# Performance work log

Measured on AMD Instinct MI355X. Metric: run time of the kernel, lower is better.

## Reference

```python
import jax, jax.numpy as jnp
import numpy as np

T, B, F, H, O = 512, 1024, 16, 32, 8  # seq_len, batch, input_size, hidden, classes


def setup_inputs() -> dict:
    key = jax.random.key(0)
    ks = jax.random.split(key, 11)
    s = 1.0 / np.sqrt(H)  # PyTorch LSTM/Linear uniform init scale
    u = lambda k, shp: jax.random.uniform(k, shp, jnp.float32, -s, s)
    return {
        "x": jax.random.normal(ks[0], (T, B, F), jnp.float32),
        "W_ih_f": u(ks[1], (4 * H, F)),
        "W_hh_f": u(ks[2], (4 * H, H)),
        "b_f": u(ks[3], (4 * H,)),  # combined b_ih + b_hh
        "W_ih_b": u(ks[4], (4 * H, F)),
        "W_hh_b": u(ks[5], (4 * H, H)),
        "b_b": u(ks[6], (4 * H,)),
        "W_fc_h": u(ks[7], (O, 2 * H)),
        "b_fc_h": u(ks[8], (O,)),
        "W_fc_o": jax.random.uniform(ks[9], (O, B * O), jnp.float32, -1 / np.sqrt(B * O), 1 / np.sqrt(B * O)),
        "b_fc_o": u(ks[10], (O,)),
    }


def _lstm_final_hidden(x, W_ih, W_hh, b):
    """Run one LSTM direction over x:(T,B,F); return final hidden h:(B,H)."""
    h_dim = W_hh.shape[1]
    # precompute input contribution for all timesteps: (T, B, 4H)
    gates_x = jnp.einsum('tbf,gf->tbg', x, W_ih) + b

    def step(carry, gx):
        h, c = carry
        g = gx + h @ W_hh.T  # (B, 4H), PyTorch gate order i,f,g,o
        i, f, gg, o = jnp.split(g, 4, axis=-1)
        c = jax.nn.sigmoid(f) * c + jax.nn.sigmoid(i) * jnp.tanh(gg)
        h = jax.nn.sigmoid(o) * jnp.tanh(c)
        return (h, c), None

    bsz = x.shape[1]
    init = (jnp.zeros((bsz, h_dim), x.dtype), jnp.zeros((bsz, h_dim), x.dtype))
    (h, _), _ = jax.lax.scan(step, init, gates_x)
    return h


def reference(x, W_ih_f, W_hh_f, b_f, W_ih_b, W_hh_b, b_b,
              W_fc_h, b_fc_h, W_fc_o, b_fc_o):
    h_fwd = _lstm_final_hidden(x, W_ih_f, W_hh_f, b_f)          # hidden_state[-2]
    h_bwd = _lstm_final_hidden(x[::-1], W_ih_b, W_hh_b, b_b)    # hidden_state[-1]
    hidden = jnp.concatenate([h_fwd, h_bwd], axis=1)            # (B, 2H)
    hidden_fc = hidden @ W_fc_h.T + b_fc_h                      # (B, O)
    flat = hidden_fc.reshape(-1)                                # (B*O,) == flat_dim
    out = W_fc_o @ flat + b_fc_o                                # (O,)
    return jax.nn.softmax(out)
```

## Files before the change

kernel.cpp:

```cpp
#include <hip/hip_runtime.h>

#define TT 512
#define BB 1024
#define FF 16
#define HH 32
#define OO 8
#define CH 16
#define NC (TT / CH)
#define NG 128

typedef _Float16 f16;
typedef f16 v2h __attribute__((ext_vector_type(2)));
typedef f16 v4h __attribute__((ext_vector_type(4)));
typedef f16 v8h __attribute__((ext_vector_type(8)));
typedef float f32x4 __attribute__((ext_vector_type(4)));
typedef int   v2i  __attribute__((ext_vector_type(2)));

__device__ __forceinline__ float rcp_fast(float x) { return __builtin_amdgcn_rcpf(x); }
__device__ __forceinline__ float sigm2(float y) {
    return rcp_fast(1.0f + __builtin_amdgcn_exp2f(-y));
}
__device__ __forceinline__ float fdot2(v2h a, v2h b, float c) {
    return __builtin_amdgcn_fdot2(a, b, c, false);
}
__device__ __forceinline__ v2h i2h(int s) { return __builtin_bit_cast(v2h, s); }

__device__ __forceinline__ float xhalf_swap(float v) {
#if __has_builtin(__builtin_amdgcn_permlane32_swap)
    int pi = __float_as_int(v);
    v2i sw = __builtin_amdgcn_permlane32_swap(pi, pi, false, false);
    return __int_as_float(sw.x);
#else
    return __shfl_xor(v, 32);
#endif
}

#define LSTEP(tt, S)                                                           \
  {                                                                            \
    const int xm = ((tt) & 7) << 2;                                            \
    const float gx0 = gxc##S[(tt) * NG + (r0 ^ xm)];                           \
    const float gx1 = gxc##S[(tt) * NG + (r1 ^ xm)];                           \
    float B0 = fdot2(i2h(hs##S[0]), w0h[0], pb0);                              \
    float B1 = fdot2(i2h(hs##S[0]), w1h[0], pb1);                              \
    float C0 = fdot2(i2h(hs##S[8]), w0h[8], gx0);                              \
    float C1 = fdot2(i2h(hs##S[8]), w1h[8], gx1);                              \
    _Pragma("unroll")                                                          \
    for (int j = 1; j < 8; ++j) {                                              \
      B0 = fdot2(i2h(hs##S[j]),     w0h[j],     B0);                           \
      B1 = fdot2(i2h(hs##S[j]),     w1h[j],     B1);                           \
      C0 = fdot2(i2h(hs##S[8 + j]), w0h[8 + j], C0);                           \
      C1 = fdot2(i2h(hs##S[8 + j]), w1h[8 + j], C1);                           \
    }                                                                          \
    const float g0 = B0 + C0;                                                  \
    const float g1 = B1 + C1;                                                  \
    const float s0 = sigm2(g0);                         \
    const float s1 = fmaf(sigm2(g1), pm, pa);           \
    const float prod = s0 * s1;                                                \
    const float recv = xhalf_swap(prod);                                       \
    c##S = fmaf(s0, c##S, recv);                         \
    const float th = fmaf(2.0f, sigm2(L2E2 * c##S), -1.0f);                    \
    h##S = s1 * th;                                        \
    const int hn = __builtin_amdgcn_mov_dpp(__float_as_int(h##S),              \
                                            0xB1, 0xF, 0xF, true);             \
    auto pk = __builtin_amdgcn_cvt_pkrtz(h##S, __int_as_float(hn));            \
    const int pki = __builtin_bit_cast(int, pk);                               \
    _Pragma("unroll")                                                          \
    for (int m = 0; m < HH / 2; ++m)                                           \
      hs##S[m] = __builtin_amdgcn_readlane(pki, 32 + 2 * m);                   \
  }

__global__ __launch_bounds__(64, 1)
void lstm_seq_kernel(const float* __restrict__ x,
                     const float* __restrict__ Wih_f, const float* __restrict__ Whh_f,
                     const float* __restrict__ b_f,
                     const float* __restrict__ Wih_b, const float* __restrict__ Whh_b,
                     const float* __restrict__ b_b,
                     float* __restrict__ hidden)
{
    const int bid  = blockIdx.x;
    const int dir  = bid >> 9;
    const int bbA  = (bid & 511) * 2;
    const int bbB  = bbA + 1;
    const int lane = threadIdx.x;
    const int hi   = lane >> 5;
    const int kk   = lane & 31;

    const float* __restrict__ Wih  = dir ? Wih_b : Wih_f;
    const float* __restrict__ Whh  = dir ? Whh_b : Whh_f;
    const float* __restrict__ bias = dir ? b_b   : b_f;

    const float LOG2E = 1.4426950408889634f;
    const float L2E2  = 2.0f * LOG2E;

    const int r0 = kk + hi * HH;
    const int r1 = r0 + 2 * HH;
    const float sc0 = LOG2E;
    const float sc1 = hi ? LOG2E : L2E2;
    const float pm = hi ? 1.0f : 2.0f;
    const float pa = hi ? 0.0f : -1.0f;

    v2h w0h[HH / 2], w1h[HH / 2];
#pragma unroll
    for (int q = 0; q < HH / 4; ++q) {
        float4 a = ((const float4*)(Whh + r0 * HH))[q];
        w0h[2*q]   = (v2h){(f16)(a.x * sc0), (f16)(a.y * sc0)};
        w0h[2*q+1] = (v2h){(f16)(a.z * sc0), (f16)(a.w * sc0)};
        float4 b2 = ((const float4*)(Whh + r1 * HH))[q];
        w1h[2*q]   = (v2h){(f16)(b2.x * sc1), (f16)(b2.y * sc1)};
        w1h[2*q+1] = (v2h){(f16)(b2.z * sc1), (f16)(b2.w * sc1)};
    }
    const float pb0 = bias[r0] * sc0;
    const float pb1 = bias[r1] * sc1;

    v8h awx[8];
#pragma unroll
    for (int T = 0; T < 8; ++T) {
        v8h t = {(f16)0,(f16)0,(f16)0,(f16)0,(f16)0,(f16)0,(f16)0,(f16)0};
        if (lane < 32) {
            const int gate = T * 16 + (lane & 15);
            const float sc = (gate >= 64 && gate < 96) ? L2E2 : LOG2E;
            const float* wrow = Wih + gate * FF + (lane >> 4) * 8;
#pragma unroll
            for (int j = 0; j < 8; ++j) t[j] = (f16)(wrow[j] * sc);
        }
        awx[T] = t;
    }

    __shared__ __align__(16) f16   xsbA[2 * CH * FF], xsbB[2 * CH * FF];
    __shared__ __align__(16) float gxbA[2 * CH * NG], gxbB[2 * CH * NG];

    const int sl = lane >> 2;
    const int wl = lane & 3;
    const int t0 = dir ? (TT - 1 - sl) : sl;
    const float* xpA = x + (size_t)t0 * (BB * FF) + (size_t)bbA * FF + wl * 4;
    const float* xpB = x + (size_t)t0 * (BB * FF) + (size_t)bbB * FF + wl * 4;
    const ptrdiff_t dstep = (dir ? -(ptrdiff_t)CH : (ptrdiff_t)CH) * (BB * FF);

    const int mst = lane & 15;
    const int mq  = (lane >> 4) * 4;
    const int mxr = (mst & 7) << 2;
    const int bsel = (lane & 15) * FF + (lane >> 4) * 8;

    {
        float4 fA = *(const float4*)xpA;
        float4 fB = *(const float4*)xpB;
        *(v4h*)(xsbA + sl * FF + wl * 4) =
            (v4h){(f16)fA.x, (f16)fA.y, (f16)fA.z, (f16)fA.w};
        *(v4h*)(xsbB + sl * FF + wl * 4) =
            (v4h){(f16)fB.x, (f16)fB.y, (f16)fB.z, (f16)fB.w};
    }
    xpA += dstep; xpB += dstep;
    {
        v8h bxA = {(f16)0,(f16)0,(f16)0,(f16)0,(f16)0,(f16)0,(f16)0,(f16)0};
        v8h bxB = bxA;
        if (lane < 32) { bxA = *(const v8h*)(xsbA + bsel);
                         bxB = *(const v8h*)(xsbB + bsel); }
        float* gwA = gxbA + mst * NG;
        float* gwB = gxbB + mst * NG;
#pragma unroll
        for (int T = 0; T < 8; ++T) {
            f32x4 aA = __builtin_amdgcn_mfma_f32_16x16x32_f16(
                awx[T], bxA, (f32x4){0.f, 0.f, 0.f, 0.f}, 0, 0, 0);
            f32x4 aB = __builtin_amdgcn_mfma_f32_16x16x32_f16(
                awx[T], bxB, (f32x4){0.f, 0.f, 0.f, 0.f}, 0, 0, 0);
            *(f32x4*)(gwA + ((mq + T * 16) ^ mxr)) = aA;
            *(f32x4*)(gwB + ((mq + T * 16) ^ mxr)) = aB;
        }
    }
    float4 nfA = *(const float4*)xpA;  xpA += dstep;
    float4 nfB = *(const float4*)xpB;  xpB += dstep;

    float cA = 0.0f, hA = 0.0f, cB = 0.0f, hB = 0.0f;
    int hsA[HH / 2], hsB[HH / 2];
#pragma unroll
    for (int m = 0; m < HH / 2; ++m) { hsA[m] = 0; hsB[m] = 0; }

    for (int ci = 0; ci < NC; ++ci) {
        const int bufc = ci & 1;
        const int bufn = bufc ^ 1;
        const bool more = (ci + 1 < NC);

        v8h bxA = {(f16)0,(f16)0,(f16)0,(f16)0,(f16)0,(f16)0,(f16)0,(f16)0};
        v8h bxB = bxA;
        if (more) {
            *(v4h*)(xsbA + bufn * (CH * FF) + sl * FF + wl * 4) =
                (v4h){(f16)nfA.x, (f16)nfA.y, (f16)nfA.z, (f16)nfA.w};
            *(v4h*)(xsbB + bufn * (CH * FF) + sl * FF + wl * 4) =
                (v4h){(f16)nfB.x, (f16)nfB.y, (f16)nfB.z, (f16)nfB.w};
            if (lane < 32) {
                bxA = *(const v8h*)(xsbA + bufn * (CH * FF) + bsel);
                bxB = *(const v8h*)(xsbB + bufn * (CH * FF) + bsel);
            }
            if (ci + 2 < NC) {
                nfA = *(const float4*)xpA;  xpA += dstep;
                nfB = *(const float4*)xpB;  xpB += dstep;
            }
        }

        const float* gxcA = gxbA + bufc * (CH * NG);
        const float* gxcB = gxbB + bufc * (CH * NG);

#pragma unroll
        for (int tt = 0; tt < 12; ++tt) { LSTEP(tt, A) LSTEP(tt, B) }

        if (more) {
            float* gwA = gxbA + bufn * (CH * NG) + mst * NG;
            float* gwB = gxbB + bufn * (CH * NG) + mst * NG;
#pragma unroll
            for (int T = 0; T < 8; ++T) {
                f32x4 aA = __builtin_amdgcn_mfma_f32_16x16x32_f16(
                    awx[T], bxA, (f32x4){0.f, 0.f, 0.f, 0.f}, 0, 0, 0);
                f32x4 aB = __builtin_amdgcn_mfma_f32_16x16x32_f16(
                    awx[T], bxB, (f32x4){0.f, 0.f, 0.f, 0.f}, 0, 0, 0);
                *(f32x4*)(gwA + ((mq + T * 16) ^ mxr)) = aA;
                *(f32x4*)(gwB + ((mq + T * 16) ^ mxr)) = aB;
            }
        }

#pragma unroll
        for (int tt = 12; tt < CH; ++tt) { LSTEP(tt, A) LSTEP(tt, B) }
    }

    if (hi) {
        hidden[(size_t)bbA * 64 + dir * HH + kk] = hA;
        hidden[(size_t)bbB * 64 + dir * HH + kk] = hB;
    }
}

__global__ __launch_bounds__(256)
void fc_partial_kernel(const float* __restrict__ hidden,
                       const float* __restrict__ Wfh, const float* __restrict__ bfh,
                       const float* __restrict__ Wfo,
                       float* __restrict__ partials)
{
    __shared__ float wsh[OO * 64];
    const int tid = threadIdx.x;
    for (int i = tid; i < OO * 64; i += 256) wsh[i] = Wfh[i];
    __syncthreads();

    const int r   = tid >> 3;
    const int o   = tid & 7;
    const int row = blockIdx.x * 32 + r;

    const float* hrow = hidden + (size_t)row * 64;
    float acc = bfh[o];
#pragma unroll
    for (int j = 0; j < 64; ++j) acc += hrow[j] * wsh[o * 64 + j];

    const int fidx = blockIdx.x * 256 + tid;

    float pv[OO];
#pragma unroll
    for (int o2 = 0; o2 < OO; ++o2) pv[o2] = Wfo[(size_t)o2 * (BB * OO) + fidx] * acc;

    __shared__ float red[4][OO];
#pragma unroll
    for (int o2 = 0; o2 < OO; ++o2) {
        float v = pv[o2];
        for (int off = 32; off > 0; off >>= 1) v += __shfl_down(v, off);
        if ((tid & 63) == 0) red[tid >> 6][o2] = v;
    }
    __syncthreads();
    if (tid < OO) {
        partials[blockIdx.x * OO + tid] =
            red[0][tid] + red[1][tid] + red[2][tid] + red[3][tid];
    }
}

__global__ void finalize_kernel(const float* __restrict__ partials,
                                const float* __restrict__ bfo,
                                float* __restrict__ out)
{
    __shared__ float s[OO];
    const int tid = threadIdx.x;
    if (tid < OO) {
        float acc = bfo[tid];
        for (int b = 0; b < 32; ++b) acc += partials[b * OO + tid];
        s[tid] = acc;
    }
    __syncthreads();
    if (tid == 0) {
        float m = s[0];
        for (int i = 1; i < OO; ++i) m = fmaxf(m, s[i]);
        float e[OO], sum = 0.0f;
        for (int i = 0; i < OO; ++i) { e[i] = expf(s[i] - m); sum += e[i]; }
        for (int i = 0; i < OO; ++i) out[i] = e[i] / sum;
    }
}

extern "C" void kernel_launch(void* const* d_in, const int* in_sizes, int n_in,
                              void* d_out, int out_size, void* d_ws, size_t ws_size,
                              hipStream_t stream) {
    const float* x     = (const float*)d_in[0];
    const float* Wih_f = (const float*)d_in[1];
    const float* Whh_f = (const float*)d_in[2];
    const float* b_f   = (const float*)d_in[3];
    const float* Wih_b = (const float*)d_in[4];
    const float* Whh_b = (const float*)d_in[5];
    const float* b_b   = (const float*)d_in[6];
    const float* Wfh   = (const float*)d_in[7];
    const float* bfh   = (const float*)d_in[8];
    const float* Wfo   = (const float*)d_in[9];
    const float* bfo   = (const float*)d_in[10];

    float* hidden   = (float*)d_ws;
    float* partials = hidden + (size_t)BB * 64;

    lstm_seq_kernel<<<BB, 64, 0, stream>>>(x, Wih_f, Whh_f, b_f,
                                           Wih_b, Whh_b, b_b, hidden);
    fc_partial_kernel<<<32, 256, 0, stream>>>(hidden, Wfh, bfh, Wfo, partials);
    finalize_kernel<<<1, 64, 0, stream>>>(partials, bfo, (float*)d_out);
}
```

Baseline: 189.9 us.

## Software-pipeline LSTM step by splitting dot products from activations across steps

The per-step LSTM macro is split into a DOTS phase (recurrent fdot2 products plus the gate input) and an ACT phase (sigmoid/tanh, cell update, hidden broadcast). The loop now issues step t's activation, then step t+1's dot products, interleaving the two independent batch streams A and B, with a prologue for step 0 and a cross-chunk handoff at the chunk boundary. The intent is to expose more independent work so the latency of the activation chain of one stream hides behind the dot products of the other. It adds live registers for the carried gate values and more complex control around the chunk boundary and the MFMA input-projection placement.

```diff
diff --git a/kernel.cpp b/kernel.cpp
--- a/kernel.cpp
+++ b/kernel.cpp
@@ -35,11 +35,11 @@
 #endif
 }
 
-#define LSTEP(tt, S)                                                           \
+#define DOTS(S, gxp, tt)                                                       \
   {                                                                            \
     const int xm = ((tt) & 7) << 2;                                            \
-    const float gx0 = gxc##S[(tt) * NG + (r0 ^ xm)];                           \
-    const float gx1 = gxc##S[(tt) * NG + (r1 ^ xm)];                           \
+    const float gx0 = (gxp)[(tt) * NG + (r0 ^ xm)];                            \
+    const float gx1 = (gxp)[(tt) * NG + (r1 ^ xm)];                            \
     float B0 = fdot2(i2h(hs##S[0]), w0h[0], pb0);                              \
     float B1 = fdot2(i2h(hs##S[0]), w1h[0], pb1);                              \
     float C0 = fdot2(i2h(hs##S[8]), w0h[8], gx0);                              \
@@ -51,10 +51,14 @@
       C0 = fdot2(i2h(hs##S[8 + j]), w0h[8 + j], C0);                           \
       C1 = fdot2(i2h(hs##S[8 + j]), w1h[8 + j], C1);                           \
     }                                                                          \
-    const float g0 = B0 + C0;                                                  \
-    const float g1 = B1 + C1;                                                  \
-    const float s0 = sigm2(g0);                         \
-    const float s1 = fmaf(sigm2(g1), pm, pa);           \
+    g##S##0 = B0 + C0;                                                         \
+    g##S##1 = B1 + C1;                                                         \
+  }
+
+#define ACT(S)                                                                 \
+  {                                                                            \
+    const float s0 = sigm2(g##S##0);                    \
+    const float s1 = fmaf(sigm2(g##S##1), pm, pa);      \
     const float prod = s0 * s1;                                                \
     const float recv = xhalf_swap(prod);                                       \
     c##S = fmaf(s0, c##S, recv);                         \
@@ -171,9 +175,13 @@
     float4 nfB = *(const float4*)xpB;  xpB += dstep;
 
     float cA = 0.0f, hA = 0.0f, cB = 0.0f, hB = 0.0f;
+    float gA0, gA1, gB0, gB1;
     int hsA[HH / 2], hsB[HH / 2];
 #pragma unroll
     for (int m = 0; m < HH / 2; ++m) { hsA[m] = 0; hsB[m] = 0; }
+
+    DOTS(A, gxbA, 0)
+    DOTS(B, gxbB, 0)
 
     for (int ci = 0; ci < NC; ++ci) {
         const int bufc = ci & 1;
@@ -199,26 +207,32 @@
 
         const float* gxcA = gxbA + bufc * (CH * NG);
         const float* gxcB = gxbB + bufc * (CH * NG);
-
-#pragma unroll
-        for (int tt = 0; tt < 12; ++tt) { LSTEP(tt, A) LSTEP(tt, B) }
-
-        if (more) {
-            float* gwA = gxbA + bufn * (CH * NG) + mst * NG;
-            float* gwB = gxbB + bufn * (CH * NG) + mst * NG;
-#pragma unroll
-            for (int T = 0; T < 8; ++T) {
-                f32x4 aA = __builtin_amdgcn_mfma_f32_16x16x32_f16(
-                    awx[T], bxA, (f32x4){0.f, 0.f, 0.f, 0.f}, 0, 0, 0);
-                f32x4 aB = __builtin_amdgcn_mfma_f32_16x16x32_f16(
-                    awx[T], bxB, (f32x4){0.f, 0.f, 0.f, 0.f}, 0, 0, 0);
-                *(f32x4*)(gwA + ((mq + T * 16) ^ mxr)) = aA;
-                *(f32x4*)(gwB + ((mq + T * 16) ^ mxr)) = aB;
+        const float* gxnA = gxbA + bufn * (CH * NG);
+        const float* gxnB = gxbB + bufn * (CH * NG);
+
+#pragma unroll
+        for (int tt = 0; tt < CH; ++tt) {
+            ACT(A)
+            if (tt < CH - 1)      { DOTS(A, gxcA, tt + 1) }
+            else if (more)        { DOTS(A, gxnA, 0) }
+            ACT(B)
+            if (tt < CH - 1)      { DOTS(B, gxcB, tt + 1) }
+            else if (more)        { DOTS(B, gxnB, 0) }
+
+            if (tt == 11 && more) {
+                float* gwA = gxbA + bufn * (CH * NG) + mst * NG;
+                float* gwB = gxbB + bufn * (CH * NG) + mst * NG;
+#pragma unroll
+                for (int T = 0; T < 8; ++T) {
+                    f32x4 aA = __builtin_amdgcn_mfma_f32_16x16x32_f16(
+                        awx[T], bxA, (f32x4){0.f, 0.f, 0.f, 0.f}, 0, 0, 0);
+                    f32x4 aB = __builtin_amdgcn_mfma_f32_16x16x32_f16(
+                        awx[T], bxB, (f32x4){0.f, 0.f, 0.f, 0.f}, 0, 0, 0);
+                    *(f32x4*)(gwA + ((mq + T * 16) ^ mxr)) = aA;
+                    *(f32x4*)(gwB + ((mq + T * 16) ^ mxr)) = aB;
+                }
             }
         }
-
-#pragma unroll
-        for (int tt = 12; tt < CH; ++tt) { LSTEP(tt, A) LSTEP(tt, B) }
     }
 
     if (hi) {
```

Measured after the change: 185.7 us. 2.2% less time.
